# Optimization experiments

Hardware: AMD Instinct MI355X
Metric: run time of the kernel (lower is better)

Reference implementation:

```python
import jax, jax.numpy as jnp
import numpy as np

B, N, D = 2, 4096, 1024
DS = 1024           # state_dim (defaults to embed_dim)
H = 4096            # mlp hidden = int(embed_dim * 4.0)
EPS = 1e-5


def _layernorm(x, w, b):
    mu = jnp.mean(x, axis=-1, keepdims=True)
    var = jnp.mean((x - mu) ** 2, axis=-1, keepdims=True)
    return (x - mu) * jax.lax.rsqrt(var + EPS) * w + b


def _selective_scan(deltaA, deltaB_u):
    # deltaA: (B, N, 1), deltaB_u: (B, N, DS). Recurrence h_i = dA_i * h + dBu_i.
    def step(h, inp):
        dA, dBu = inp           # (B,1), (B,DS)
        h = dA * h + dBu
        return h, h
    h0 = jnp.zeros((deltaB_u.shape[0], deltaB_u.shape[2]), deltaB_u.dtype)
    _, ys = jax.lax.scan(step, h0,
                         (jnp.swapaxes(deltaA, 0, 1), jnp.swapaxes(deltaB_u, 0, 1)))
    return jnp.swapaxes(ys, 0, 1)   # (B, N, DS)


def _forward(x, norm1_w, norm1_b, gate_w, gate_b, state_w, state_b,
             out_w, out_b, norm2_w, norm2_b, mlp_w1, mlp_b1, mlp_w2, mlp_b2):
    xn = _layernorm(x, norm1_w, norm1_b)
    g = xn @ gate_w + gate_b                       # (B,N,2D)
    gate, gate_gate = jnp.split(g, 2, axis=-1)
    gate = jax.nn.silu(gate)
    gate_gate = jax.nn.silu(gate_gate)
    u = (xn * gate) @ state_w + state_b            # (B,N,DS)
    Bm = gate_gate @ state_w + state_b             # (B,N,DS)
    # A = -ones(DS) -> delta*A = -delta broadcast over DS; keep (B,N,1)
    delta = jax.nn.softplus(jnp.mean(xn @ state_w + state_b, axis=-1, keepdims=True))
    deltaA = jnp.exp(-delta)                       # (B,N,1)
    deltaB_u = delta * Bm * u                      # (B,N,DS)
    # C = ones -> y_i = C_i * h_i = h_i
    y = _selective_scan(deltaA, deltaB_u)
    ssm_out = y @ out_w + out_b
    x = x + ssm_out
    x2 = _layernorm(x, norm2_w, norm2_b)
    mlp = jax.nn.gelu(x2 @ mlp_w1 + mlp_b1, approximate=False) @ mlp_w2 + mlp_b2
    return x + mlp


def setup_inputs() -> dict:
    key = jax.random.key(0)
    ks = jax.random.split(key, 12)
    s = 0.02
    p = lambda k, shape: jax.random.normal(k, shape, jnp.float32) * s
    return {
        "x": jax.random.normal(ks[0], (B, N, D), jnp.float32),
        "norm1_w": jnp.ones((D,), jnp.float32), "norm1_b": jnp.zeros((D,), jnp.float32),
        "gate_w": p(ks[1], (D, 2 * D)), "gate_b": p(ks[2], (2 * D,)),
        "state_w": p(ks[3], (D, DS)), "state_b": p(ks[4], (DS,)),
        "out_w": p(ks[5], (DS, D)), "out_b": p(ks[6], (D,)),
        "norm2_w": jnp.ones((D,), jnp.float32), "norm2_b": jnp.zeros((D,), jnp.float32),
        "mlp_w1": p(ks[7], (D, H)), "mlp_b1": p(ks[8], (H,)),
        "mlp_w2": p(ks[9], (H, D)), "mlp_b2": p(ks[10], (D,)),
    }


def reference(x, norm1_w, norm1_b, gate_w, gate_b, state_w, state_b,
              out_w, out_b, norm2_w, norm2_b, mlp_w1, mlp_b1, mlp_w2, mlp_b2):
    return _forward(x, norm1_w, norm1_b, gate_w, gate_b, state_w, state_b,
                    out_w, out_b, norm2_w, norm2_b, mlp_w1, mlp_b1, mlp_w2, mlp_b2)
```

## Files before the change

### kernel.cpp

```cpp
#include <hip/hip_runtime.h>
#include <hip/hip_bf16.h>
#include <math.h>

#define B_   2
#define N_   4096
#define D_   1024
#define DS_  1024
#define HID_ 4096
#define ROWS (B_ * N_)

#define CHK 128
#define TCH 32

typedef __attribute__((ext_vector_type(8))) short bf16x8;
typedef __attribute__((ext_vector_type(4))) float f32x4;

#define ASG __attribute__((address_space(1)))
#define AS3 __attribute__((address_space(3)))

__device__ __forceinline__ float bf2f(unsigned short u) {
  union { float f; unsigned int i; } v; v.i = ((unsigned int)u) << 16; return v.f;
}
__device__ __forceinline__ unsigned short f2bf(float f) {
  union { float f; unsigned int i; } v; v.f = f;
  unsigned int r = v.i + 0x7fffu + ((v.i >> 16) & 1u);
  return (unsigned short)(r >> 16);
}

__global__ void means_kernel(const float* __restrict__ W, const float* __restrict__ bvec,
                             float* __restrict__ swmean, float* __restrict__ sbmean) {
  __shared__ float sm[4];
  int bid = blockIdx.x, t = threadIdx.x;
  const float* src = (bid < D_) ? (W + (size_t)bid * DS_) : bvec;
  float s = 0.f;
  for (int j = t; j < DS_; j += 256) s += src[j];
  for (int o = 32; o; o >>= 1) s += __shfl_down(s, o);
  if ((t & 63) == 0) sm[t >> 6] = s;
  __syncthreads();
  if (t == 0) {
    float r = (sm[0] + sm[1] + sm[2] + sm[3]) * (1.f / DS_);
    if (bid < D_) swmean[bid] = r; else sbmean[0] = r;
  }
}

__global__ void transpose_bf16_kernel(const float* __restrict__ W, unsigned short* __restrict__ WT,
                                      int K, int N) {
  __shared__ float tile[32][33];
  int tx = threadIdx.x & 31, ty = threadIdx.x >> 5;
  int bn = blockIdx.x * 32, bk = blockIdx.y * 32;
  for (int i = ty; i < 32; i += 8)
    tile[i][tx] = W[(size_t)(bk + i) * N + bn + tx];
  __syncthreads();
  for (int i = ty; i < 32; i += 8)
    WT[(size_t)(bn + i) * K + bk + tx] = f2bf(tile[tx][i]);
}

template<bool WITH_DELTA>
__global__ void ln_kernel(const float* __restrict__ x, const float* __restrict__ w,
                          const float* __restrict__ bb, unsigned short* __restrict__ out_bf,
                          const float* __restrict__ swmean, const float* __restrict__ sbmean,
                          float* __restrict__ delta) {
  __shared__ float sm[8];
  __shared__ float bc[2];
  int row = blockIdx.x, t = threadIdx.x;
  const float* xr = x + (size_t)row * D_;
  float4 xv = ((const float4*)xr)[t];
  float s  = xv.x + xv.y + xv.z + xv.w;
  float sq = xv.x * xv.x + xv.y * xv.y + xv.z * xv.z + xv.w * xv.w;
  for (int o = 32; o; o >>= 1) { s += __shfl_down(s, o); sq += __shfl_down(sq, o); }
  if ((t & 63) == 0) { sm[t >> 6] = s; sm[4 + (t >> 6)] = sq; }
  __syncthreads();
  if (t == 0) {
    float ts = sm[0] + sm[1] + sm[2] + sm[3];
    float tq = sm[4] + sm[5] + sm[6] + sm[7];
    float mu = ts * (1.f / D_);
    float var = tq * (1.f / D_) - mu * mu;
    bc[0] = mu; bc[1] = rsqrtf(var + 1e-5f);
  }
  __syncthreads();
  float mu = bc[0], rs = bc[1];
  float4 wv = ((const float4*)w)[t];
  float4 bv = ((const float4*)bb)[t];
  float n0 = (xv.x - mu) * rs * wv.x + bv.x;
  float n1 = (xv.y - mu) * rs * wv.y + bv.y;
  float n2 = (xv.z - mu) * rs * wv.z + bv.z;
  float n3 = (xv.w - mu) * rs * wv.w + bv.w;
  ushort4 o4; o4.x = f2bf(n0); o4.y = f2bf(n1); o4.z = f2bf(n2); o4.w = f2bf(n3);
  ((ushort4*)(out_bf + (size_t)row * D_))[t] = o4;
  if (WITH_DELTA) {
    float4 sw = ((const float4*)swmean)[t];
    float d = n0 * sw.x + n1 * sw.y + n2 * sw.z + n3 * sw.w;
    for (int o = 32; o; o >>= 1) d += __shfl_down(d, o);
    if ((t & 63) == 0) sm[t >> 6] = d;
    __syncthreads();
    if (t == 0) {
      float z = sm[0] + sm[1] + sm[2] + sm[3] + sbmean[0];
      delta[row] = (z > 15.f) ? z : log1pf(__expf(z));
    }
  }
}


#define BAR __builtin_amdgcn_s_barrier()

#define RD_A(TAU, H) { const char* ab_ = smem + ((((TAU)&1)*2+(H))<<14); \
  _Pragma("unroll") for (int mm_ = 0; mm_ < MB_H; ++mm_) \
  _Pragma("unroll") for (int ks_ = 0; ks_ < 2; ++ks_) { \
    int r_ = wr*(16*MB_H) + mm_*16 + l15; \
    int by_ = r_*128 + ks_*64 + kq16; by_ ^= ((by_>>7)&7)<<4; \
    af[mm_][ks_] = *(const bf16x8*)(ab_ + by_); } }

#define RD_B(TAU, H, DST) { const char* bb_ = smemB + ((((TAU)&1)*2+(H)))*SB; \
  _Pragma("unroll") for (int nn_ = 0; nn_ < NB_H; ++nn_) \
  _Pragma("unroll") for (int ks_ = 0; ks_ < 2; ++ks_) { \
    int r_ = wc*(16*NB_H) + nn_*16 + l15; \
    int by_ = r_*128 + ks_*64 + kq16; by_ ^= ((by_>>7)&7)<<4; \
    DST[nn_][ks_] = *(const bf16x8*)(bb_ + by_); } }

#define MFMAQ(QA, QB, BF) { __builtin_amdgcn_s_setprio(1); \
  _Pragma("unroll") for (int m_ = 0; m_ < MB_H; ++m_) \
  _Pragma("unroll") for (int n_ = 0; n_ < NB_H; ++n_) \
  _Pragma("unroll") for (int k_ = 0; k_ < 2; ++k_) \
    acc[(QA)*MB_H+m_][(QB)*NB_H+n_] = __builtin_amdgcn_mfma_f32_16x16x32_bf16( \
        af[m_][k_], BF[n_][k_], acc[(QA)*MB_H+m_][(QB)*NB_H+n_], 0, 0, 0); \
  __builtin_amdgcn_s_setprio(0); }

template<int BN, int EPI>
__global__ __launch_bounds__(512, 2) void gemm8p(
    const unsigned short* __restrict__ A1p, int lda1, int M1,
    const unsigned short* __restrict__ A2p, int lda2,
    const unsigned short* __restrict__ BT, const float* __restrict__ bias,
    void* __restrict__ Cout, const float* __restrict__ res,
    int N, int K, int nbx, void* __restrict__ Cout2) {
  constexpr int WN   = (BN == 256) ? 4 : 2;
  constexpr int MB_H = (BN == 256) ? 4 : 2;
  constexpr int NB_H = 2;
  constexpr int MF   = 2 * MB_H;
  constexpr int LB   = BN / 128;
  constexpr int SB   = (BN / 2) * 64 * 2;
  __shared__ char smem[65536 + 4 * SB];
  char* smemB = smem + 65536;

  const int nwg = gridDim.x;
  int bid = blockIdx.x;
  int wg = (bid & 7) * (nwg >> 3) + (bid >> 3);
  const int bx = wg % nbx, by = wg / nbx;
  const int mbase = by * 256, nbase = bx * BN;

  const int tid = threadIdx.x;
  const int lane = tid & 63, wid = tid >> 6;
  const int wr = wid / WN, wc = wid % WN;
  const int l15 = lane & 15, kq16 = (lane >> 4) * 16;
  const int wvoff16 = wid << 10;

  const unsigned short* Ause; int ldaU;
  if (mbase < M1) { Ause = A1p + (size_t)mbase * lda1; ldaU = lda1; }
  else            { Ause = A2p + (size_t)(mbase - M1) * lda2; ldaU = lda2; }

  int L0 = tid * 16;        int b0 = L0 ^ (((L0 >> 7) & 7) << 4);
  int L1 = 8192 + tid * 16; int b1 = L1 ^ (((L1 >> 7) & 7) << 4);
  const unsigned short* pA0 = Ause + (size_t)(b0 >> 7) * ldaU + ((b0 & 127) >> 1);
  const unsigned short* pA1 = Ause + (size_t)(b1 >> 7) * ldaU + ((b1 & 127) >> 1);
  const unsigned short* pB0 = BT + (size_t)(nbase + (b0 >> 7)) * K + ((b0 & 127) >> 1);
  const unsigned short* pB1 = BT + (size_t)(nbase + (b1 >> 7)) * K + ((b1 & 127) >> 1);

  auto stageA = [&](int tau, int h, bool en) {
    if (!en) return;
    char* l0 = smem + (((tau & 1) * 2 + h) << 14) + wvoff16;
    const unsigned short* g0 = pA0 + (size_t)h * 128 * ldaU + tau * 64;
    const unsigned short* g1 = pA1 + (size_t)h * 128 * ldaU + tau * 64;
    __builtin_amdgcn_global_load_lds((const ASG void*)g0, (AS3 void*)l0, 16, 0, 0);
    __builtin_amdgcn_global_load_lds((const ASG void*)g1, (AS3 void*)(l0 + 8192), 16, 0, 0);
  };
  auto stageB = [&](int tau, int h, bool en) {
    if (!en) return;
    char* l0 = smemB + ((tau & 1) * 2 + h) * SB + wvoff16;
    const unsigned short* g0 = pB0 + (size_t)h * (BN / 2) * K + tau * 64;
    __builtin_amdgcn_global_load_lds((const ASG void*)g0, (AS3 void*)l0, 16, 0, 0);
    if constexpr (LB == 2) {
      const unsigned short* g1 = pB1 + (size_t)h * (BN / 2) * K + tau * 64;
      __builtin_amdgcn_global_load_lds((const ASG void*)g1, (AS3 void*)(l0 + 8192), 16, 0, 0);
    }
  };
  auto vm_steady = [&]() {
    if constexpr (BN == 256) { asm volatile("s_waitcnt vmcnt(6)" ::: "memory"); }
    else                     { asm volatile("s_waitcnt vmcnt(5)" ::: "memory"); }
  };

  f32x4 acc[MF][4];
#pragma unroll
  for (int m = 0; m < MF; ++m)
#pragma unroll
    for (int n = 0; n < 4; ++n) acc[m][n] = (f32x4){0.f, 0.f, 0.f, 0.f};
  bf16x8 af[MB_H][2], bq0[NB_H][2], bq1[NB_H][2];

  const int NT = K >> 6, NI = NT >> 1;

  stageA(0, 0, true); stageB(0, 0, true); stageA(0, 1, true); stageB(0, 1, true);
  stageA(1, 0, true); stageB(1, 0, true); stageA(1, 1, true);
  vm_steady();
  BAR;

#pragma unroll 1
  for (int i = 0; i < NI; ++i) {
    const int t0 = 2 * i;
    const bool st = (i < NI - 1);
    stageB(t0 + 1, 1, true); RD_A(t0, 0); RD_B(t0, 0, bq0);
    BAR; MFMAQ(0, 0, bq0); BAR;
    stageA(t0 + 2, 0, st); RD_B(t0, 1, bq1);
    BAR; MFMAQ(0, 1, bq1); BAR;
    stageB(t0 + 2, 0, st); RD_A(t0, 1);
    BAR; MFMAQ(1, 1, bq1); BAR;
    stageA(t0 + 2, 1, st);
    if (st) { vm_steady(); } else { asm volatile("s_waitcnt vmcnt(0)" ::: "memory"); }
    BAR; MFMAQ(1, 0, bq0); BAR;
    stageB(t0 + 2, 1, st); RD_A(t0 + 1, 0); RD_B(t0 + 1, 0, bq0);
    BAR; MFMAQ(0, 0, bq0); BAR;
    stageA(t0 + 3, 0, st); RD_B(t0 + 1, 1, bq1);
    BAR; MFMAQ(0, 1, bq1); BAR;
    stageB(t0 + 3, 0, st); RD_A(t0 + 1, 1);
    BAR; MFMAQ(1, 1, bq1); BAR;
    stageA(t0 + 3, 1, st);
    if (st) vm_steady();
    BAR; MFMAQ(1, 0, bq0); BAR;
  }

#pragma unroll
  for (int mb = 0; mb < MF; ++mb) {
    int row = mbase + wr * (16 * MB_H) + (mb % MB_H) * 16 + (mb / MB_H) * 128 + (lane >> 4) * 4;
#pragma unroll
    for (int nb = 0; nb < 4; ++nb) {
      int col = nbase + wc * (16 * NB_H) + (nb % NB_H) * 16 + (nb / NB_H) * (BN / 2) + l15;
      float bc = bias[col];
#pragma unroll
      for (int r = 0; r < 4; ++r) {
        float v = acc[mb][nb][r] + bc;
        size_t off = (size_t)(row + r) * N + col;
        if (EPI == 1) {
          v = v / (1.f + __expf(-v));
          ((unsigned short*)Cout)[off] = f2bf(v);
        } else if (EPI == 2) {
          ((unsigned short*)Cout)[off] = f2bf(v);
        } else if (EPI == 3) {
          ((float*)Cout)[off] = v + res[off];
        } else if (EPI == 4) {
          float tt = v * (0.7978845608f + 0.0356774081f * v * v);
          v = v / (1.f + __expf(-2.f * tt));
          ((unsigned short*)Cout)[off] = f2bf(v);
        } else if (EPI == 5) {
          float s = v / (1.f + __expf(-v));
          if (col < 1024) {
            size_t o1 = (size_t)(row + r) * 1024 + col;
            float xv = bf2f(((const unsigned short*)res)[o1]);
            ((unsigned short*)Cout)[o1] = f2bf(s * xv);
          } else {
            size_t o2 = (size_t)(row + r) * 1024 + (col - 1024);
            ((unsigned short*)Cout2)[o2] = f2bf(s);
          }
        }
      }
    }
  }
}

__global__ void ew_dbu_kernel(const unsigned short* __restrict__ u,
                              const unsigned short* __restrict__ bm,
                              const float* __restrict__ delta,
                              unsigned short* __restrict__ dbu) {
  size_t i8 = ((size_t)blockIdx.x * 256 + threadIdx.x) * 8;
  size_t row = i8 >> 10;
  float dl = delta[row];
  uint4 uv = *(const uint4*)(u + i8);
  uint4 bv = *(const uint4*)(bm + i8);
  const unsigned short* us = (const unsigned short*)&uv;
  const unsigned short* bs = (const unsigned short*)&bv;
  uint4 ov; unsigned short* o = (unsigned short*)&ov;
#pragma unroll
  for (int j = 0; j < 8; ++j) o[j] = f2bf(dl * bf2f(us[j]) * bf2f(bs[j]));
  *(uint4*)(dbu + i8) = ov;
}

__global__ void scan_a_kernel(const unsigned short* __restrict__ dbu,
                              const float* __restrict__ delta,
                              float* __restrict__ hend, float* __restrict__ S) {
  int blk = blockIdx.x;
  int b = blk / CHK, c = blk % CHK;
  int ch = threadIdx.x;
  const unsigned short* p = dbu + ((size_t)(b * N_ + c * TCH)) * DS_ + ch;
  const float* dp = delta + b * N_ + c * TCH;
  float h = 0.f, dsum = 0.f;
#pragma unroll 4
  for (int t = 0; t < TCH; ++t) {
    float dl = dp[t];
    h = __expf(-dl) * h + bf2f(p[(size_t)t * DS_]);
    dsum += dl;
  }
  hend[(size_t)blk * DS_ + ch] = h;
  if (ch == 0) S[blk] = dsum;
}

__global__ void scan_combine_kernel(const float* __restrict__ hend, const float* __restrict__ S,
                                    float* __restrict__ carryin) {
  int b = blockIdx.x, ch = threadIdx.x;
  float carry = 0.f;
  for (int c = 0; c < CHK; ++c) {
    size_t o = (size_t)(b * CHK + c) * DS_ + ch;
    carryin[o] = carry;
    carry = __expf(-S[b * CHK + c]) * carry + hend[o];
  }
}

__global__ void scan_b_kernel(const unsigned short* __restrict__ dbu,
                              const float* __restrict__ delta,
                              const float* __restrict__ carryin,
                              unsigned short* __restrict__ y) {
  int blk = blockIdx.x;
  int b = blk / CHK, c = blk % CHK;
  int ch = threadIdx.x;
  size_t base = ((size_t)(b * N_ + c * TCH)) * DS_ + ch;
  const float* dp = delta + b * N_ + c * TCH;
  float h = carryin[(size_t)blk * DS_ + ch];
#pragma unroll 4
  for (int t = 0; t < TCH; ++t) {
    h = __expf(-dp[t]) * h + bf2f(dbu[base + (size_t)t * DS_]);
    y[base + (size_t)t * DS_] = f2bf(h);
  }
}

extern "C" void kernel_launch(void* const* d_in, const int* in_sizes, int n_in,
                              void* d_out, int out_size, void* d_ws, size_t ws_size,
                              hipStream_t stream) {
  const float* x       = (const float*)d_in[0];
  const float* n1w     = (const float*)d_in[1];
  const float* n1b     = (const float*)d_in[2];
  const float* gate_w  = (const float*)d_in[3];
  const float* gate_b  = (const float*)d_in[4];
  const float* state_w = (const float*)d_in[5];
  const float* state_b = (const float*)d_in[6];
  const float* out_w   = (const float*)d_in[7];
  const float* out_b   = (const float*)d_in[8];
  const float* n2w     = (const float*)d_in[9];
  const float* n2b     = (const float*)d_in[10];
  const float* mlp_w1  = (const float*)d_in[11];
  const float* mlp_b1  = (const float*)d_in[12];
  const float* mlp_w2  = (const float*)d_in[13];
  const float* mlp_b2  = (const float*)d_in[14];
  float* outp = (float*)d_out;

  char* w = (char*)d_ws;
  size_t off = 0;
  auto alloc = [&](size_t bytes) { char* p = w + off; off += (bytes + 255) & ~(size_t)255; return p; };

  unsigned short* gate_wT  = (unsigned short*)alloc((size_t)2048 * 1024 * 2);
  unsigned short* state_wT = (unsigned short*)alloc((size_t)1024 * 1024 * 2);
  unsigned short* out_wT   = (unsigned short*)alloc((size_t)1024 * 1024 * 2);
  unsigned short* w1T      = (unsigned short*)alloc((size_t)4096 * 1024 * 2);
  unsigned short* w2T      = (unsigned short*)alloc((size_t)1024 * 4096 * 2);
  float* swmean  = (float*)alloc(D_ * 4);
  float* sbmean  = (float*)alloc(256);
  float* delta   = (float*)alloc((size_t)ROWS * 4);
  float* hend    = (float*)alloc((size_t)B_ * CHK * DS_ * 4);
  float* carryin = (float*)alloc((size_t)B_ * CHK * DS_ * 4);
  float* S       = (float*)alloc((size_t)B_ * CHK * 4);
  unsigned short* xn = (unsigned short*)alloc((size_t)ROWS * D_ * 2);
  unsigned short* gs = (unsigned short*)alloc((size_t)ROWS * HID_ * 2);
  unsigned short* xg = (unsigned short*)alloc((size_t)ROWS * D_ * 2);
  float* x1          = (float*)alloc((size_t)ROWS * D_ * 4);

  unsigned short* dbu   = xn;
  unsigned short* gsil2 = gs;
  unsigned short* h1    = gs;
  unsigned short* y     = xg;
  unsigned short* x2    = xg;
  unsigned short* u     = (unsigned short*)x1;
  unsigned short* bm    = u + (size_t)ROWS * D_;

  means_kernel<<<D_ + 1, 256, 0, stream>>>(state_w, state_b, swmean, sbmean);
  transpose_bf16_kernel<<<dim3(2048 / 32, 1024 / 32), 256, 0, stream>>>(gate_w, gate_wT, 1024, 2048);
  transpose_bf16_kernel<<<dim3(1024 / 32, 1024 / 32), 256, 0, stream>>>(state_w, state_wT, 1024, 1024);
  transpose_bf16_kernel<<<dim3(1024 / 32, 1024 / 32), 256, 0, stream>>>(out_w, out_wT, 1024, 1024);
  transpose_bf16_kernel<<<dim3(4096 / 32, 1024 / 32), 256, 0, stream>>>(mlp_w1, w1T, 1024, 4096);
  transpose_bf16_kernel<<<dim3(1024 / 32, 4096 / 32), 256, 0, stream>>>(mlp_w2, w2T, 4096, 1024);

  ln_kernel<true><<<ROWS, 256, 0, stream>>>(x, n1w, n1b, xn, swmean, sbmean, delta);

  const int BIG = 1 << 30;
  gemm8p<256, 5><<<256, 512, 0, stream>>>(xn, 1024, BIG, xn, 1024,
                                          gate_wT, gate_b, xg, (const float*)xn, 2048, 1024, 8, gsil2);
  gemm8p<256, 2><<<256, 512, 0, stream>>>(xg, 1024, 8192, gsil2, 1024,
                                          state_wT, state_b, u, nullptr, 1024, 1024, 4, nullptr);
  ew_dbu_kernel<<<(ROWS * D_) / 8 / 256, 256, 0, stream>>>(u, bm, delta, dbu);

  scan_a_kernel<<<B_ * CHK, 1024, 0, stream>>>(dbu, delta, hend, S);
  scan_combine_kernel<<<B_, 1024, 0, stream>>>(hend, S, carryin);
  scan_b_kernel<<<B_ * CHK, 1024, 0, stream>>>(dbu, delta, carryin, y);

  gemm8p<128, 3><<<256, 512, 0, stream>>>(y, 1024, BIG, y, 1024,
                                          out_wT, out_b, x1, x, 1024, 1024, 8, nullptr);
  ln_kernel<false><<<ROWS, 256, 0, stream>>>(x1, n2w, n2b, x2, nullptr, nullptr, nullptr);
  gemm8p<256, 4><<<512, 512, 0, stream>>>(x2, 1024, BIG, x2, 1024,
                                          w1T, mlp_b1, h1, nullptr, 4096, 1024, 16, nullptr);
  gemm8p<128, 3><<<256, 512, 0, stream>>>(h1, 4096, BIG, h1, 4096,
                                          w2T, mlp_b2, outp, x1, 1024, 4096, 8, nullptr);
}
```

Baseline: 392.9 us.

## Stage GEMM epilogue through LDS for coalesced stores; fuse dBu into scans

The GEMM epilogue now writes activated results into shared memory with an XOR swizzle, then reads them back so each thread issues 16-byte coalesced global stores and residual loads, instead of scattered 2- or 4-byte stores per element. Separately, the standalone delta*Bm*u elementwise kernel is removed and the product is recomputed inside both scan passes, which drops one full intermediate tensor write and read. The cost is extra barriers and LDS traffic in the epilogue, plus reading two input tensors in each scan pass instead of one, and the epilogue relies on enough shared memory being available for a half-tile.

```diff
diff --git a/kernel.cpp b/kernel.cpp
--- a/kernel.cpp
+++ b/kernel.cpp
@@ -225,74 +225,84 @@
     BAR; MFMAQ(1, 0, bq0); BAR;
   }
 
-#pragma unroll
-  for (int mb = 0; mb < MF; ++mb) {
-    int row = mbase + wr * (16 * MB_H) + (mb % MB_H) * 16 + (mb / MB_H) * 128 + (lane >> 4) * 4;
-#pragma unroll
-    for (int nb = 0; nb < 4; ++nb) {
-      int col = nbase + wc * (16 * NB_H) + (nb % NB_H) * 16 + (nb / NB_H) * (BN / 2) + l15;
-      float bc = bias[col];
-#pragma unroll
-      for (int r = 0; r < 4; ++r) {
-        float v = acc[mb][nb][r] + bc;
-        size_t off = (size_t)(row + r) * N + col;
-        if (EPI == 1) {
-          v = v / (1.f + __expf(-v));
-          ((unsigned short*)Cout)[off] = f2bf(v);
-        } else if (EPI == 2) {
-          ((unsigned short*)Cout)[off] = f2bf(v);
-        } else if (EPI == 3) {
-          ((float*)Cout)[off] = v + res[off];
-        } else if (EPI == 4) {
-          float tt = v * (0.7978845608f + 0.0356774081f * v * v);
-          v = v / (1.f + __expf(-2.f * tt));
-          ((unsigned short*)Cout)[off] = f2bf(v);
-        } else if (EPI == 5) {
-          float s = v / (1.f + __expf(-v));
-          if (col < 1024) {
-            size_t o1 = (size_t)(row + r) * 1024 + col;
-            float xv = bf2f(((const unsigned short*)res)[o1]);
-            ((unsigned short*)Cout)[o1] = f2bf(s * xv);
-          } else {
-            size_t o2 = (size_t)(row + r) * 1024 + (col - 1024);
-            ((unsigned short*)Cout2)[o2] = f2bf(s);
+  constexpr int EOUT_E = (EPI == 3) ? 4 : 2;
+  constexpr int RB = BN * EOUT_E;
+  const int rl_rb = tid >> 2;
+  const int cb_rb = (tid & 3) * 16;
+  const int r0 = (lane >> 4) * 4;
+
+#pragma unroll 1
+  for (int h = 0; h < 2; ++h) {
+    __syncthreads();
+#pragma unroll
+    for (int mm = 0; mm < MB_H; ++mm) {
+      int rl = wr * (16 * MB_H) + mm * 16 + r0;
+#pragma unroll
+      for (int nb = 0; nb < 4; ++nb) {
+        int cl = wc * (16 * NB_H) + (nb & 1) * 16 + (nb >> 1) * (BN / 2) + l15;
+        float bc = bias[nbase + cl];
+#pragma unroll
+        for (int r = 0; r < 4; ++r) {
+          float v = acc[h * MB_H + mm][nb][r] + bc;
+          if (EPI == 1 || EPI == 5) {
+            v = v / (1.f + __expf(-v));
+          } else if (EPI == 4) {
+            float tt = v * (0.7978845608f + 0.0356774081f * v * v);
+            v = v / (1.f + __expf(-2.f * tt));
           }
+          int byo = (rl + r) * RB + cl * EOUT_E;
+          byo ^= ((rl + r) & 7) << 4;
+          if (EPI == 3) *(float*)(smem + byo) = v;
+          else          *(unsigned short*)(smem + byo) = f2bf(v);
         }
       }
     }
-  }
-}
-
-__global__ void ew_dbu_kernel(const unsigned short* __restrict__ u,
+    __syncthreads();
+    const int grow = mbase + h * 128 + rl_rb;
+#pragma unroll
+    for (int j = 0; j < RB / 64; ++j) {
+      int byo = rl_rb * RB + cb_rb + j * 64;
+      byo ^= (rl_rb & 7) << 4;
+      uint4 d = *(const uint4*)(smem + byo);
+      int ce = (cb_rb + j * 64) / EOUT_E;
+      if (EPI == 3) {
+        float4 f = *(const float4*)&d;
+        const float4 rv = *(const float4*)(res + (size_t)grow * N + nbase + ce);
+        f.x += rv.x; f.y += rv.y; f.z += rv.z; f.w += rv.w;
+        *(float4*)((float*)Cout + (size_t)grow * N + nbase + ce) = f;
+      } else if (EPI == 5) {
+        if (nbase < 1024) {
+          uint4 xv = *(const uint4*)((const unsigned short*)res + (size_t)grow * 1024 + nbase + ce);
+          unsigned short* dp = (unsigned short*)&d;
+          const unsigned short* xp = (const unsigned short*)&xv;
+#pragma unroll
+          for (int q = 0; q < 8; ++q) dp[q] = f2bf(bf2f(dp[q]) * bf2f(xp[q]));
+          *(uint4*)((unsigned short*)Cout + (size_t)grow * 1024 + nbase + ce) = d;
+        } else {
+          *(uint4*)((unsigned short*)Cout2 + (size_t)grow * 1024 + (nbase - 1024) + ce) = d;
+        }
+      } else {
+        *(uint4*)((unsigned short*)Cout + (size_t)grow * N + nbase + ce) = d;
+      }
+    }
+  }
+}
+
+__global__ void scan_a_kernel(const unsigned short* __restrict__ u,
                               const unsigned short* __restrict__ bm,
-                              const float* __restrict__ delta,
-                              unsigned short* __restrict__ dbu) {
-  size_t i8 = ((size_t)blockIdx.x * 256 + threadIdx.x) * 8;
-  size_t row = i8 >> 10;
-  float dl = delta[row];
-  uint4 uv = *(const uint4*)(u + i8);
-  uint4 bv = *(const uint4*)(bm + i8);
-  const unsigned short* us = (const unsigned short*)&uv;
-  const unsigned short* bs = (const unsigned short*)&bv;
-  uint4 ov; unsigned short* o = (unsigned short*)&ov;
-#pragma unroll
-  for (int j = 0; j < 8; ++j) o[j] = f2bf(dl * bf2f(us[j]) * bf2f(bs[j]));
-  *(uint4*)(dbu + i8) = ov;
-}
-
-__global__ void scan_a_kernel(const unsigned short* __restrict__ dbu,
                               const float* __restrict__ delta,
                               float* __restrict__ hend, float* __restrict__ S) {
   int blk = blockIdx.x;
   int b = blk / CHK, c = blk % CHK;
   int ch = threadIdx.x;
-  const unsigned short* p = dbu + ((size_t)(b * N_ + c * TCH)) * DS_ + ch;
+  size_t base = ((size_t)(b * N_ + c * TCH)) * DS_ + ch;
   const float* dp = delta + b * N_ + c * TCH;
   float h = 0.f, dsum = 0.f;
 #pragma unroll 4
   for (int t = 0; t < TCH; ++t) {
     float dl = dp[t];
-    h = __expf(-dl) * h + bf2f(p[(size_t)t * DS_]);
+    float du = dl * bf2f(u[base + (size_t)t * DS_]) * bf2f(bm[base + (size_t)t * DS_]);
+    h = __expf(-dl) * h + du;
     dsum += dl;
   }
   hend[(size_t)blk * DS_ + ch] = h;
@@ -310,7 +320,8 @@
   }
 }
 
-__global__ void scan_b_kernel(const unsigned short* __restrict__ dbu,
+__global__ void scan_b_kernel(const unsigned short* __restrict__ u,
+                              const unsigned short* __restrict__ bm,
                               const float* __restrict__ delta,
                               const float* __restrict__ carryin,
                               unsigned short* __restrict__ y) {
@@ -322,7 +333,9 @@
   float h = carryin[(size_t)blk * DS_ + ch];
 #pragma unroll 4
   for (int t = 0; t < TCH; ++t) {
-    h = __expf(-dp[t]) * h + bf2f(dbu[base + (size_t)t * DS_]);
+    float dl = dp[t];
+    float du = dl * bf2f(u[base + (size_t)t * DS_]) * bf2f(bm[base + (size_t)t * DS_]);
+    h = __expf(-dl) * h + du;
     y[base + (size_t)t * DS_] = f2bf(h);
   }
 }
@@ -367,7 +380,6 @@
   unsigned short* xg = (unsigned short*)alloc((size_t)ROWS * D_ * 2);
   float* x1          = (float*)alloc((size_t)ROWS * D_ * 4);
 
-  unsigned short* dbu   = xn;
   unsigned short* gsil2 = gs;
   unsigned short* h1    = gs;
   unsigned short* y     = xg;
@@ -389,11 +401,10 @@
                                           gate_wT, gate_b, xg, (const float*)xn, 2048, 1024, 8, gsil2);
   gemm8p<256, 2><<<256, 512, 0, stream>>>(xg, 1024, 8192, gsil2, 1024,
                                           state_wT, state_b, u, nullptr, 1024, 1024, 4, nullptr);
-  ew_dbu_kernel<<<(ROWS * D_) / 8 / 256, 256, 0, stream>>>(u, bm, delta, dbu);
-
-  scan_a_kernel<<<B_ * CHK, 1024, 0, stream>>>(dbu, delta, hend, S);
+
+  scan_a_kernel<<<B_ * CHK, 1024, 0, stream>>>(u, bm, delta, hend, S);
   scan_combine_kernel<<<B_, 1024, 0, stream>>>(hend, S, carryin);
-  scan_b_kernel<<<B_ * CHK, 1024, 0, stream>>>(dbu, delta, carryin, y);
+  scan_b_kernel<<<B_ * CHK, 1024, 0, stream>>>(u, bm, delta, carryin, y);
 
   gemm8p<128, 3><<<256, 512, 0, stream>>>(y, 1024, BIG, y, 1024,
                                           out_wT, out_b, x1, x, 1024, 1024, 8, nullptr);
```

Result: slower. 503.9 us (+28.3%).
